# Kernel optimization log

Measured on AMD Instinct MI355X. Metric: run time of the kernel, lower is better.

The kernel has to match this reference:

```python
import jax, jax.numpy as jnp
import numpy as np

PHM_DIM = 4
IN_FEATS = 2048
OUT_FEATS = 8192
TOKENS = 8192


def setup_inputs() -> dict:
    key = jax.random.key(0)
    k_x, k_rule, k_w = jax.random.split(key, 3)
    x = jax.random.normal(k_x, (TOKENS, IN_FEATS), dtype=jnp.float32)
    # c_init='normal', std=0.01
    phm_rule = 0.01 * jax.random.normal(k_rule, (PHM_DIM, PHM_DIM, PHM_DIM), dtype=jnp.float32)
    # w_init='normal', std=phm_init_range=1e-4 (scaled up here for numerics of the test)
    W = 1e-4 * jax.random.normal(k_w, (PHM_DIM, IN_FEATS // PHM_DIM, OUT_FEATS // PHM_DIM), dtype=jnp.float32)
    b = jnp.zeros((OUT_FEATS,), dtype=jnp.float32)
    return {"x": x, "phm_rule": phm_rule, "W": W, "b": b}


def reference(x, phm_rule, W, b):
    # H = sum_i kron(phm_rule[i], W[i])  with shape (phm_dim*in_per, phm_dim*out_per)
    # kron(A, B)[a*in_per + c, k*out_per + p] = A[a, k] * B[c, p]
    d, in_per, out_per = W.shape
    H = jnp.einsum('iak,icp->acKp'.replace('K', 'k'), phm_rule, W)  # (d, in_per, d, out_per)
    H = H.reshape(d * in_per, d * out_per)
    y = x @ H + b
    return y
```

## Files before the change

kernel.cpp:

```cpp
#include <hip/hip_runtime.h>
#include <stdint.h>

#define PHM      4
#define IN_FEATS 2048
#define OUT_FEATS 8192
#define TOKENS   8192
#define IN_PER   512
#define OUT_PER  2048

typedef __attribute__((ext_vector_type(8)))  short short8;
typedef __attribute__((ext_vector_type(4)))  float f32x4;
typedef __attribute__((ext_vector_type(8)))  unsigned short u16x8;

__device__ inline unsigned short f2bf(float f) {
    unsigned int u = __builtin_bit_cast(unsigned int, f);
    u += 0x7fffu + ((u >> 16) & 1u);
    return (unsigned short)(u >> 16);
}

__global__ void cvt_x_kernel(const float* __restrict__ x,
                             unsigned short* __restrict__ xb) {
    int i = blockIdx.x * blockDim.x + threadIdx.x;
    const float4* x4 = (const float4*)x;
    float4 v0 = x4[2 * i];
    float4 v1 = x4[2 * i + 1];
    u16x8 o;
    o[0] = f2bf(v0.x); o[1] = f2bf(v0.y); o[2] = f2bf(v0.z); o[3] = f2bf(v0.w);
    o[4] = f2bf(v1.x); o[5] = f2bf(v1.y); o[6] = f2bf(v1.z); o[7] = f2bf(v1.w);
    *(u16x8*)(xb + 8 * (size_t)i) = o;
}

__global__ void build_ht_kernel(const float* __restrict__ rule,
                                const float* __restrict__ W,
                                unsigned short* __restrict__ Ht)
{
    __shared__ float lds[PHM][32][65];
    const int tid = threadIdx.x;
    const int c0 = blockIdx.x * 32;
    const int p0 = blockIdx.y * 64;

    #pragma unroll
    for (int it = 0; it < 32; ++it) {
        int idx = it * 256 + tid;
        int pp = idx & 63;
        int cc = (idx >> 6) & 31;
        int i  = idx >> 11;
        lds[i][cc][pp] = W[((size_t)(i * IN_PER + c0 + cc)) * OUT_PER + p0 + pp];
    }
    __syncthreads();

    const int pp = tid >> 2;
    const int j0 = (tid & 3) * 8;
    float w[PHM][8];
    #pragma unroll
    for (int i = 0; i < PHM; ++i)
        #pragma unroll
        for (int j = 0; j < 8; ++j)
            w[i][j] = lds[i][j0 + j][pp];

    #pragma unroll
    for (int a = 0; a < PHM; ++a) {
        #pragma unroll
        for (int kq = 0; kq < PHM; ++kq) {
            float r0 = rule[(0 * PHM + a) * PHM + kq];
            float r1 = rule[(1 * PHM + a) * PHM + kq];
            float r2 = rule[(2 * PHM + a) * PHM + kq];
            float r3 = rule[(3 * PHM + a) * PHM + kq];
            u16x8 o;
            #pragma unroll
            for (int j = 0; j < 8; ++j) {
                float v = r0 * w[0][j] + r1 * w[1][j] + r2 * w[2][j] + r3 * w[3][j];
                o[j] = f2bf(v);
            }
            size_t n = (size_t)(kq * OUT_PER + p0 + pp);
            *(u16x8*)(Ht + n * IN_FEATS + a * IN_PER + c0 + j0) = o;
        }
    }
}

#define BM 256
#define BN 256
#define BK 64
#define NT (IN_FEATS / BK)

__device__ inline void gload16(const unsigned short* g, unsigned short* l) {
    __builtin_amdgcn_global_load_lds(
        (const __attribute__((address_space(1))) unsigned int*)g,
        (__attribute__((address_space(3))) unsigned int*)l,
        16, 0, 0);
}

#define WAITV(N) asm volatile("s_waitcnt vmcnt(" #N ")" ::: "memory")
#define LGKM0    asm volatile("s_waitcnt lgkmcnt(0)" ::: "memory")
#define FENCE    asm volatile("" ::: "memory")
#define SBAR     do { FENCE; __builtin_amdgcn_s_barrier(); FENCE; } while (0)

__global__ __launch_bounds__(512, 2) void gemm_bt_kernel(
    const unsigned short* __restrict__ A,
    const unsigned short* __restrict__ B,
    const float* __restrict__ bias,
    float* __restrict__ C)
{
    constexpr int N = OUT_FEATS, K = IN_FEATS;
    __shared__ unsigned short LDS[65536];

    const int tid  = threadIdx.x;
    const int wave = tid >> 6;
    const int lane = tid & 63;
    const int lm16 = lane & 15;
    const int l47  = lane >> 4;

    const int bn = blockIdx.x;
    const int bm = blockIdx.y;

    const int wm = (wave >> 2) * 64;
    const int wn = (wave & 3) * 32;

    const int aB  = (wm + lm16) * 64;
    const int bB  = 16384 + (wn + lm16) * 64;
    const int sc0 = ((l47      ^ (lane & 7))) * 8;
    const int sc1 = (((4 + l47) ^ (lane & 7))) * 8;

    const int srow = tid >> 3;
    const int schk = (lane & 7) ^ ((lane >> 3) & 7);
    const unsigned short* AgS = A + (size_t)(bm * BM + srow) * K + schk * 8;
    const unsigned short* BgS = B + (size_t)(bn * BN + srow) * K + schk * 8;

    #define STG_A(db, h, T) do { \
        gload16(AgS + (size_t)((h) * 128)      * K + (T) * 64, LDS + (db) + (h) * 8192        + wave * 512); \
        gload16(AgS + (size_t)((h) * 128 + 64) * K + (T) * 64, LDS + (db) + (h) * 8192 + 4096 + wave * 512); } while (0)
    #define STG_B(db, h, T) do { \
        gload16(BgS + (size_t)((h) * 128)      * K + (T) * 64, LDS + 16384 + (db) + (h) * 8192        + wave * 512); \
        gload16(BgS + (size_t)((h) * 128 + 64) * K + (T) * 64, LDS + 16384 + (db) + (h) * 8192 + 4096 + wave * 512); } while (0)

    #define RD_A(D, FB) do { _Pragma("unroll") \
        for (int ff = 0; ff < 4; ++ff) { \
            a[ff][0] = *(const short8*)(LDS + (D) + aB + (FB) + ff * 1024 + sc0); \
            a[ff][1] = *(const short8*)(LDS + (D) + aB + (FB) + ff * 1024 + sc1); } } while (0)
    #define RD_B01(D) do { _Pragma("unroll") \
        for (int g = 0; g < 2; ++g) { \
            b[g][0] = *(const short8*)(LDS + (D) + bB + g * 1024 + sc0); \
            b[g][1] = *(const short8*)(LDS + (D) + bB + g * 1024 + sc1); } } while (0)
    #define RD_B23(D) do { _Pragma("unroll") \
        for (int g = 0; g < 2; ++g) { \
            b[2 + g][0] = *(const short8*)(LDS + (D) + bB + 8192 + g * 1024 + sc0); \
            b[2 + g][1] = *(const short8*)(LDS + (D) + bB + 8192 + g * 1024 + sc1); } } while (0)

    #define MM(FB, GB) do { _Pragma("unroll") \
        for (int k2 = 0; k2 < 2; ++k2) { _Pragma("unroll") \
            for (int ff = 0; ff < 4; ++ff) { _Pragma("unroll") \
                for (int g = 0; g < 2; ++g) \
                    acc[(FB) + ff][(GB) + g] = __builtin_amdgcn_mfma_f32_16x16x32_bf16( \
                        a[ff][k2], b[(GB) + g][k2], acc[(FB) + ff][(GB) + g], 0, 0, 0); } } } while (0)

    #define PH_MID do { SBAR; LGKM0; __builtin_amdgcn_sched_barrier(0); \
                        __builtin_amdgcn_s_setprio(1); } while (0)
    #define PH_END do { __builtin_amdgcn_s_setprio(0); SBAR; } while (0)

    STG_A(0, 0, 0);  STG_B(0, 0, 0);  STG_B(0, 1, 0);  STG_A(0, 1, 0);
    STG_A(32768, 0, 1);  STG_B(32768, 0, 1);  STG_B(32768, 1, 1);
    WAITV(8);
    SBAR;

    f32x4 acc[8][4] = {};
    short8 a[4][2], b[4][2];

    #pragma unroll 1
    for (int j = 0; j < NT / 2 - 1; ++j) {
        const int t2 = 2 * j + 2, t3 = 2 * j + 3;
        WAITV(8); RD_A(0, 0); RD_B01(0); STG_A(32768, 1, 2 * j + 1);
        PH_MID; MM(0, 0); PH_END;
        WAITV(8); RD_B23(0); STG_A(0, 0, t2);
        PH_MID; MM(0, 2); PH_END;
        WAITV(8); RD_A(0, 8192); STG_B(0, 0, t2);
        PH_MID; MM(4, 0); PH_END;
        WAITV(8); STG_B(0, 1, t2);
        PH_MID; MM(4, 2); PH_END;
        WAITV(8); RD_A(32768, 0); RD_B01(32768); STG_A(0, 1, t2);
        PH_MID; MM(0, 0); PH_END;
        WAITV(8); RD_B23(32768); STG_A(32768, 0, t3);
        PH_MID; MM(0, 2); PH_END;
        WAITV(8); RD_A(32768, 8192); STG_B(32768, 0, t3);
        PH_MID; MM(4, 0); PH_END;
        WAITV(8); STG_B(32768, 1, t3);
        PH_MID; MM(4, 2); PH_END;
    }

    WAITV(8); RD_A(0, 0); RD_B01(0); STG_A(32768, 1, NT - 1);
    PH_MID; MM(0, 0); PH_END;
    WAITV(8); RD_B23(0);
    PH_MID; MM(0, 2); PH_END;
    WAITV(8); RD_A(0, 8192);
    PH_MID; MM(4, 0); PH_END;
    WAITV(4);
    PH_MID; MM(4, 2); PH_END;
    WAITV(2); RD_A(32768, 0); RD_B01(32768);
    PH_MID; MM(0, 0); PH_END;
    WAITV(0); RD_B23(32768);
    PH_MID; MM(0, 2); PH_END;
    RD_A(32768, 8192);
    PH_MID; MM(4, 0); PH_END;
    PH_MID; MM(4, 2); PH_END;

    #pragma unroll
    for (int g = 0; g < 4; ++g) {
        const int col = bn * BN + wn + (g >> 1) * 128 + (g & 1) * 16 + lm16;
        const float bv = bias[col];
        #pragma unroll
        for (int f = 0; f < 8; ++f) {
            const int row0 = bm * BM + wm + (f >> 2) * 128 + (f & 3) * 16 + l47 * 4;
            #pragma unroll
            for (int r = 0; r < 4; ++r)
                C[(size_t)(row0 + r) * N + col] = acc[f][g][r] + bv;
        }
    }
    #undef STG_A
    #undef STG_B
    #undef RD_A
    #undef RD_B01
    #undef RD_B23
    #undef MM
    #undef PH_MID
    #undef PH_END
}

extern "C" void kernel_launch(void* const* d_in, const int* in_sizes, int n_in,
                              void* d_out, int out_size, void* d_ws, size_t ws_size,
                              hipStream_t stream) {
    const float* x    = (const float*)d_in[0];
    const float* rule = (const float*)d_in[1];
    const float* W    = (const float*)d_in[2];
    const float* b    = (const float*)d_in[3];
    float* y = (float*)d_out;

    unsigned short* xb = (unsigned short*)d_ws;
    unsigned short* Ht = (unsigned short*)((char*)d_ws +
                         (size_t)TOKENS * IN_FEATS * sizeof(unsigned short));

    cvt_x_kernel<<<(TOKENS * IN_FEATS) / 8 / 256, 256, 0, stream>>>(x, xb);
    build_ht_kernel<<<dim3(IN_PER / 32, OUT_PER / 64), 256, 0, stream>>>(rule, W, Ht);
    gemm_bt_kernel<<<dim3(OUT_FEATS / BN, TOKENS / BM), 512, 0, stream>>>(xb, Ht, b, y);
}
```

Baseline: 544.8 us.

## Merge x-convert and H-build into one prep launch; relax GEMM vmcnt waits

Folds the x bf16 conversion and the Kronecker H construction into a single prep kernel whose block index selects the job, so one launch and its inter-kernel gap go away. In the GEMM main loop, the per-phase global-load waits are cut back to one wait per half-iteration with a lower outstanding count, so more global loads stay in flight during the MFMA phases. The risk is that the fewer waits no longer cover every LDS read of freshly staged data, which would give wrong results, and the prep blocks now use a shared allocation even in the convert path.

```diff
diff --git a/kernel.cpp b/kernel.cpp
--- a/kernel.cpp
+++ b/kernel.cpp
@@ -18,26 +18,32 @@
     return (unsigned short)(u >> 16);
 }
 
-__global__ void cvt_x_kernel(const float* __restrict__ x,
-                             unsigned short* __restrict__ xb) {
-    int i = blockIdx.x * blockDim.x + threadIdx.x;
-    const float4* x4 = (const float4*)x;
-    float4 v0 = x4[2 * i];
-    float4 v1 = x4[2 * i + 1];
-    u16x8 o;
-    o[0] = f2bf(v0.x); o[1] = f2bf(v0.y); o[2] = f2bf(v0.z); o[3] = f2bf(v0.w);
-    o[4] = f2bf(v1.x); o[5] = f2bf(v1.y); o[6] = f2bf(v1.z); o[7] = f2bf(v1.w);
-    *(u16x8*)(xb + 8 * (size_t)i) = o;
-}
-
-__global__ void build_ht_kernel(const float* __restrict__ rule,
-                                const float* __restrict__ W,
-                                unsigned short* __restrict__ Ht)
+#define BUILD_BLOCKS 512
+#define CVT_BLOCKS   8192
+
+__global__ void prep_kernel(const float* __restrict__ x,
+                            unsigned short* __restrict__ xb,
+                            const float* __restrict__ rule,
+                            const float* __restrict__ W,
+                            unsigned short* __restrict__ Ht)
 {
     __shared__ float lds[PHM][32][65];
     const int tid = threadIdx.x;
-    const int c0 = blockIdx.x * 32;
-    const int p0 = blockIdx.y * 64;
+
+    if (blockIdx.x >= BUILD_BLOCKS) {
+        int i = (blockIdx.x - BUILD_BLOCKS) * blockDim.x + tid;
+        const float4* x4 = (const float4*)x;
+        float4 v0 = x4[2 * i];
+        float4 v1 = x4[2 * i + 1];
+        u16x8 o;
+        o[0] = f2bf(v0.x); o[1] = f2bf(v0.y); o[2] = f2bf(v0.z); o[3] = f2bf(v0.w);
+        o[4] = f2bf(v1.x); o[5] = f2bf(v1.y); o[6] = f2bf(v1.z); o[7] = f2bf(v1.w);
+        *(u16x8*)(xb + 8 * (size_t)i) = o;
+        return;
+    }
+
+    const int c0 = (blockIdx.x & 15) * 32;
+    const int p0 = (blockIdx.x >> 4) * 64;
 
     #pragma unroll
     for (int it = 0; it < 32; ++it) {
@@ -159,7 +165,7 @@
 
     STG_A(0, 0, 0);  STG_B(0, 0, 0);  STG_B(0, 1, 0);  STG_A(0, 1, 0);
     STG_A(32768, 0, 1);  STG_B(32768, 0, 1);  STG_B(32768, 1, 1);
-    WAITV(8);
+    WAITV(6);
     SBAR;
 
     f32x4 acc[8][4] = {};
@@ -168,33 +174,33 @@
     #pragma unroll 1
     for (int j = 0; j < NT / 2 - 1; ++j) {
         const int t2 = 2 * j + 2, t3 = 2 * j + 3;
-        WAITV(8); RD_A(0, 0); RD_B01(0); STG_A(32768, 1, 2 * j + 1);
+        RD_A(0, 0); RD_B01(0); STG_A(32768, 1, 2 * j + 1);
         PH_MID; MM(0, 0); PH_END;
-        WAITV(8); RD_B23(0); STG_A(0, 0, t2);
+        RD_B23(0); STG_A(0, 0, t2);
         PH_MID; MM(0, 2); PH_END;
-        WAITV(8); RD_A(0, 8192); STG_B(0, 0, t2);
+        RD_A(0, 8192); STG_B(0, 0, t2);
         PH_MID; MM(4, 0); PH_END;
-        WAITV(8); STG_B(0, 1, t2);
+        WAITV(4); STG_B(0, 1, t2);
         PH_MID; MM(4, 2); PH_END;
-        WAITV(8); RD_A(32768, 0); RD_B01(32768); STG_A(0, 1, t2);
+        RD_A(32768, 0); RD_B01(32768); STG_A(0, 1, t2);
         PH_MID; MM(0, 0); PH_END;
-        WAITV(8); RD_B23(32768); STG_A(32768, 0, t3);
+        RD_B23(32768); STG_A(32768, 0, t3);
         PH_MID; MM(0, 2); PH_END;
-        WAITV(8); RD_A(32768, 8192); STG_B(32768, 0, t3);
+        RD_A(32768, 8192); STG_B(32768, 0, t3);
         PH_MID; MM(4, 0); PH_END;
-        WAITV(8); STG_B(32768, 1, t3);
+        WAITV(4); STG_B(32768, 1, t3);
         PH_MID; MM(4, 2); PH_END;
     }
 
-    WAITV(8); RD_A(0, 0); RD_B01(0); STG_A(32768, 1, NT - 1);
+    RD_A(0, 0); RD_B01(0); STG_A(32768, 1, NT - 1);
     PH_MID; MM(0, 0); PH_END;
-    WAITV(8); RD_B23(0);
+    RD_B23(0);
     PH_MID; MM(0, 2); PH_END;
-    WAITV(8); RD_A(0, 8192);
+    RD_A(0, 8192);
     PH_MID; MM(4, 0); PH_END;
-    WAITV(4);
+    WAITV(2);
     PH_MID; MM(4, 2); PH_END;
-    WAITV(2); RD_A(32768, 0); RD_B01(32768);
+    RD_A(32768, 0); RD_B01(32768);
     PH_MID; MM(0, 0); PH_END;
     WAITV(0); RD_B23(32768);
     PH_MID; MM(0, 2); PH_END;
@@ -237,7 +243,6 @@
     unsigned short* Ht = (unsigned short*)((char*)d_ws +
                          (size_t)TOKENS * IN_FEATS * sizeof(unsigned short));
 
-    cvt_x_kernel<<<(TOKENS * IN_FEATS) / 8 / 256, 256, 0, stream>>>(x, xb);
-    build_ht_kernel<<<dim3(IN_PER / 32, OUT_PER / 64), 256, 0, stream>>>(rule, W, Ht);
+    prep_kernel<<<BUILD_BLOCKS + CVT_BLOCKS, 256, 0, stream>>>(x, xb, rule, W, Ht);
     gemm_bt_kernel<<<dim3(OUT_FEATS / BN, TOKENS / BM), 512, 0, stream>>>(xb, Ht, b, y);
 }
```

Result: faster. 524.7 us (-3.7%).
